# Kernel tuning notes

Hardware: AMD Instinct MI355X
Metric: run time of the kernel (lower is better)

The kernel has to match this reference:

```python
import jax, jax.numpy as jnp
import numpy as np

HEAD_DIM = 256
HIDDEN = 2560
NUM_HEADS = 8
NUM_KV_HEADS = 4
INPUT_DIM = HIDDEN * 2
B, S = 2, 2048


def rotate_half(x):
    x1, x2 = x[..., : x.shape[-1] // 2], x[..., x.shape[-1] // 2 :]
    return jnp.concatenate((-x2, x1), axis=-1)


def setup_inputs() -> dict:
    key = jax.random.key(0)
    ks = jax.random.split(key, 6)
    hidden_states = jax.random.normal(ks[0], (B, S, INPUT_DIM), dtype=jnp.float32)
    # causal additive mask (0 on/below diagonal, large negative above)
    causal = jnp.tril(jnp.ones((S, S), dtype=bool))
    attention_mask = jnp.where(causal, 0.0, -1e9).astype(jnp.float32)
    attention_mask = jnp.broadcast_to(attention_mask[None, None], (B, 1, S, S))
    position_ids = jnp.broadcast_to(jnp.arange(S, dtype=jnp.int32)[None], (B, S))
    sc = 1.0 / np.sqrt(INPUT_DIM)
    Wq = jax.random.normal(ks[1], (NUM_HEADS * HEAD_DIM, INPUT_DIM), dtype=jnp.float32) * sc
    Wk = jax.random.normal(ks[2], (NUM_KV_HEADS * HEAD_DIM, INPUT_DIM), dtype=jnp.float32) * sc
    Wv = jax.random.normal(ks[3], (NUM_KV_HEADS * HEAD_DIM, INPUT_DIM), dtype=jnp.float32) * sc
    Wo = jax.random.normal(ks[4], (HIDDEN, NUM_HEADS * HEAD_DIM), dtype=jnp.float32) * (1.0 / np.sqrt(NUM_HEADS * HEAD_DIM))
    return {"hidden_states": hidden_states, "attention_mask": attention_mask,
            "position_ids": position_ids, "Wq": Wq, "Wk": Wk, "Wv": Wv, "Wo": Wo}


def reference(hidden_states, attention_mask, position_ids, Wq, Wk, Wv, Wo):
    bsz, q_len, _ = hidden_states.shape
    groups = NUM_HEADS // NUM_KV_HEADS
    q = (hidden_states @ Wq.T).reshape(bsz, q_len, NUM_HEADS, HEAD_DIM).transpose(0, 2, 1, 3)
    k = (hidden_states @ Wk.T).reshape(bsz, q_len, NUM_KV_HEADS, HEAD_DIM).transpose(0, 2, 1, 3)
    v = (hidden_states @ Wv.T).reshape(bsz, q_len, NUM_KV_HEADS, HEAD_DIM).transpose(0, 2, 1, 3)
    # RoPE (uses position_ids[0], matching the torch module)
    inv_freq = 1.0 / (10000.0 ** (jnp.arange(0, HEAD_DIM, 2, dtype=jnp.float32) / HEAD_DIM))
    freqs = position_ids[0].astype(jnp.float32)[:, None] * inv_freq[None, :]  # [S, D/2]
    emb = jnp.concatenate((freqs, freqs), axis=-1)  # [S, D]
    cos = jnp.cos(emb)[None, None].astype(q.dtype)
    sin = jnp.sin(emb)[None, None].astype(q.dtype)
    q = q * cos + rotate_half(q) * sin
    k = k * cos + rotate_half(k) * sin
    # GQA: repeat kv heads
    k = jnp.repeat(k, groups, axis=1)  # [B, H, S, D]
    v = jnp.repeat(v, groups, axis=1)
    scores = jnp.einsum("bhqd,bhkd->bhqk", q, k) / np.sqrt(HEAD_DIM)
    scores = scores + attention_mask
    attn = jax.nn.softmax(scores.astype(jnp.float32), axis=-1).astype(q.dtype)
    out = jnp.einsum("bhqk,bhkd->bhqd", attn, v)
    out = out.transpose(0, 2, 1, 3).reshape(bsz, q_len, NUM_HEADS * HEAD_DIM)
    return out @ Wo.T
```

## Files before the change

### kernel.cpp

```cpp
#include <hip/hip_runtime.h>
#include <hip/hip_bf16.h>
#include <cstdint>
#include <cstddef>

typedef __bf16 bf16;
typedef bf16 bf16x4 __attribute__((ext_vector_type(4)));
typedef bf16 bf16x8 __attribute__((ext_vector_type(8)));
typedef float f32x4 __attribute__((ext_vector_type(4)));

#define HEAD_DIM 256
#define NHEADS 8
#define NKV 4
#define BATCH 2
#define SEQ 2048
#define IND 5120
#define HID 2560
#define ROWS (BATCH*SEQ)
#define NQKV 4096
#define CHUNKS_PER_BH 80

__device__ __forceinline__ f32x4 mfma16(bf16x8 a, bf16x8 b, f32x4 c) {
  return __builtin_amdgcn_mfma_f32_16x16x32_bf16(a, b, c, 0, 0, 0);
}

__global__ void cast8(const float* __restrict__ in, bf16* __restrict__ out, int n) {
  int i = (blockIdx.x * 256 + threadIdx.x) * 8;
  if (i >= n) return;
  float4 a = *(const float4*)(in + i);
  float4 b = *(const float4*)(in + i + 4);
  bf16x8 o;
  o[0] = (bf16)a.x; o[1] = (bf16)a.y; o[2] = (bf16)a.z; o[3] = (bf16)a.w;
  o[4] = (bf16)b.x; o[5] = (bf16)b.y; o[6] = (bf16)b.z; o[7] = (bf16)b.w;
  *(bf16x8*)(out + i) = o;
}

template<typename OutT>
__global__ __launch_bounds__(512, 2) void gemm_pipe(const bf16* __restrict__ A,
                                                    const bf16* __restrict__ B,
                                                    OutT* __restrict__ C,
                                                    int M, int N, int K) {
  extern __shared__ bf16 smem[];
  const int tid = threadIdx.x;
  const int lane = tid & 63, w = tid >> 6;
  const int wm = w >> 2, wn = w & 3;
  const int l15 = lane & 15, lg = lane >> 4;
  const int gx = gridDim.x;
  const int nwg = gx * gridDim.y;
  const int id = blockIdx.y * gx + blockIdx.x;
  const int nid = (id & 7) * (nwg >> 3) + (id >> 3);
  const int m0 = (nid / gx) * 256, n0 = (nid % gx) * 256;
  const int NT = K >> 5;

  auto stage = [&](int slot, int kt) {
    bf16* sl = smem + slot * 16384;
    #pragma unroll
    for (int i = 0; i < 2; ++i) {
      int cid = i * 512 + tid;
      int row = cid >> 2;
      int sch = (cid & 3) ^ (row & 3);
      __builtin_amdgcn_global_load_lds(
        (const __attribute__((address_space(1))) void*)(A + (size_t)(m0 + row) * K + kt * 32 + sch * 8),
        (__attribute__((address_space(3))) void*)(sl + cid * 8), 16, 0, 0);
    }
    #pragma unroll
    for (int i = 0; i < 2; ++i) {
      int cid = i * 512 + tid;
      int row = cid >> 2;
      int sch = (cid & 3) ^ (row & 3);
      __builtin_amdgcn_global_load_lds(
        (const __attribute__((address_space(1))) void*)(B + (size_t)(n0 + row) * K + kt * 32 + sch * 8),
        (__attribute__((address_space(3))) void*)(sl + 8192 + cid * 8), 16, 0, 0);
    }
  };

  stage(0, 0); stage(1, 1); stage(2, 2);

  f32x4 acc[8][4] = {};
  for (int t = 0; t < NT; ++t) {
    asm volatile("s_waitcnt vmcnt(8)" ::: "memory");
    __builtin_amdgcn_s_barrier();
    const bf16* sl = smem + (t & 3) * 16384;
    bf16x8 a[8], b[4];
    #pragma unroll
    for (int mi = 0; mi < 8; ++mi) {
      int row = wm * 128 + mi * 16 + l15;
      a[mi] = *(const bf16x8*)&sl[(row * 4 + (lg ^ (row & 3))) * 8];
    }
    #pragma unroll
    for (int ni = 0; ni < 4; ++ni) {
      int row = wn * 64 + ni * 16 + l15;
      b[ni] = *(const bf16x8*)&sl[8192 + (row * 4 + (lg ^ (row & 3))) * 8];
    }
    __builtin_amdgcn_s_setprio(1);
    #pragma unroll
    for (int ni = 0; ni < 2; ++ni)
      #pragma unroll
      for (int mi = 0; mi < 8; ++mi)
        acc[mi][ni] = mfma16(a[mi], b[ni], acc[mi][ni]);
    __builtin_amdgcn_s_setprio(0);
    asm volatile("s_waitcnt lgkmcnt(0)" ::: "memory");
    __builtin_amdgcn_s_barrier();
    int kt = t + 3; if (kt > NT - 1) kt = NT - 1;
    stage((t + 3) & 3, kt);
    __builtin_amdgcn_s_setprio(1);
    #pragma unroll
    for (int ni = 2; ni < 4; ++ni)
      #pragma unroll
      for (int mi = 0; mi < 8; ++mi)
        acc[mi][ni] = mfma16(a[mi], b[ni], acc[mi][ni]);
    __builtin_amdgcn_s_setprio(0);
  }

  #pragma unroll
  for (int mi = 0; mi < 8; ++mi)
    #pragma unroll
    for (int ni = 0; ni < 4; ++ni) {
      int row = m0 + wm * 128 + mi * 16 + lg * 4;
      int col = n0 + wn * 64 + ni * 16 + l15;
      #pragma unroll
      for (int r = 0; r < 4; ++r)
        C[(size_t)(row + r) * N + col] = (OutT)acc[mi][ni][r];
    }
}

__global__ void rope_reorder(const bf16* __restrict__ QKV,
                             bf16* __restrict__ Qr, bf16* __restrict__ Kr) {
  const int row = blockIdx.x;
  const int slot = blockIdx.y;
  const int d = threadIdx.x;
  const int b = row >> 11, s = row & 2047;
  const bool isq = slot < 8;
  const int col0 = isq ? slot * HEAD_DIM : 2048 + (slot - 8) * HEAD_DIM;
  float x1 = (float)QKV[(size_t)row * NQKV + col0 + d];
  float x2 = (float)QKV[(size_t)row * NQKV + col0 + d + 128];
  float invf = exp2f((float)d * (-13.287712379549449f / 128.0f));
  float fr = (float)s * invf;
  float sn, cs;
  sincosf(fr, &sn, &cs);
  bf16* dst = isq ? (Qr + ((size_t)(b * NHEADS + slot) * SEQ + s) * HEAD_DIM)
                  : (Kr + ((size_t)(b * NKV + (slot - 8)) * SEQ + s) * HEAD_DIM);
  dst[d]       = (bf16)(x1 * cs - x2 * sn);
  dst[d + 128] = (bf16)(x2 * cs + x1 * sn);
}

__global__ void v_transpose(const bf16* __restrict__ QKV, bf16* __restrict__ VT) {
  __shared__ bf16 tile[64][66];
  const int bkv = blockIdx.y;
  const int b = bkv >> 2, kv = bkv & 3;
  const int st = blockIdx.x & 31, dt = blockIdx.x >> 5;
  const int s0 = st * 64, d0 = dt * 64;
  const int tj = threadIdx.x & 63, ti = threadIdx.x >> 6;
  for (int i = ti; i < 64; i += 4)
    tile[i][tj] = QKV[(size_t)(b * SEQ + s0 + i) * NQKV + 3072 + kv * HEAD_DIM + d0 + tj];
  __syncthreads();
  for (int i = ti; i < 64; i += 4)
    VT[((size_t)bkv * HEAD_DIM + d0 + i) * SEQ + s0 + tj] = tile[tj][i];
}

__global__ __launch_bounds__(256) void flash_attn(const bf16* __restrict__ Q,
                                                  const bf16* __restrict__ Kp,
                                                  const bf16* __restrict__ VT,
                                                  bf16* __restrict__ Opart,
                                                  float* __restrict__ ML) {
  __shared__ bf16 Ks[64 * 256];
  __shared__ bf16 Vs[256 * 64];
  __shared__ bf16 pbuf[4][16][80];

  const int tid = threadIdx.x, lane = tid & 63, w = tid >> 6;
  const int l15 = lane & 15, lg = lane >> 4;

  const int cid = blockIdx.x;
  const int bh = cid / CHUNKS_PER_BH;
  const int c  = cid - bh * CHUNKS_PER_BH;
  int qt, ki;
  if (c < 8)       { qt = c;                 ki = 0; }
  else if (c < 24) { qt = 8  + ((c - 8) >> 1);  ki = (c - 8)  & 1; }
  else if (c < 48) { qt = 16 + (c - 24) / 3;    ki = (c - 24) % 3; }
  else             { qt = 24 + ((c - 48) >> 2); ki = (c - 48) & 3; }
  const int kb0 = ki * 8;
  const int kb1 = min(kb0 + 8, qt + 1);

  const int b = bh >> 3, h = bh & 7, kvh = h >> 1;
  const int bkv = b * NKV + kvh;
  const int q0 = qt * 64 + w * 16;

  const bf16* Qb = Q + ((size_t)bh * SEQ + q0) * HEAD_DIM;
  bf16x8 qf[8];
  #pragma unroll
  for (int dc = 0; dc < 8; ++dc)
    qf[dc] = *(const bf16x8*)&Qb[l15 * HEAD_DIM + dc * 32 + lg * 8];

  f32x4 oacc[16] = {};
  float m = -1e30f, l = 0.f;

  const bf16* Ksrc = Kp + (size_t)bkv * SEQ * HEAD_DIM;
  const bf16* Vsrc = VT + (size_t)bkv * HEAD_DIM * SEQ;

  for (int kb = kb0; kb < kb1; ++kb) {
    const int kbase = kb * 64;
    __syncthreads();
    #pragma unroll
    for (int i = 0; i < 8; ++i) {
      int id = i * 256 + tid;
      int row = id >> 5, ch = id & 31;
      int sc = ch ^ (row & 7);
      __builtin_amdgcn_global_load_lds(
          (const __attribute__((address_space(1))) void*)(Ksrc + (size_t)(kbase + row) * HEAD_DIM + sc * 8),
          (__attribute__((address_space(3))) void*)(Ks + id * 8), 16, 0, 0);
    }
    #pragma unroll
    for (int i = 0; i < 8; ++i) {
      int id = i * 256 + tid;
      int row = id >> 3, ch = id & 7;
      int sc = ch ^ (row & 7);
      __builtin_amdgcn_global_load_lds(
          (const __attribute__((address_space(1))) void*)(Vsrc + (size_t)row * SEQ + kbase + sc * 8),
          (__attribute__((address_space(3))) void*)(Vs + id * 8), 16, 0, 0);
    }
    __syncthreads();

    f32x4 sacc[4] = {};
    #pragma unroll
    for (int j = 0; j < 4; ++j) {
      const bf16* kl = &Ks[(j * 16 + l15) * HEAD_DIM];
      #pragma unroll
      for (int dc = 0; dc < 8; ++dc) {
        int ch = (dc * 4 + lg) ^ (l15 & 7);
        bf16x8 kf = *(const bf16x8*)&kl[ch * 8];
        sacc[j] = mfma16(kf, qf[dc], sacc[j]);
      }
    }

    float px[4][4];
    const bool need_mask = (kbase + 63 > q0);
    #pragma unroll
    for (int j = 0; j < 4; ++j)
      #pragma unroll
      for (int r = 0; r < 4; ++r) {
        float v = sacc[j][r] * 0.0625f;
        if (need_mask) {
          int kcol = kbase + j * 16 + lg * 4 + r;
          v = (kcol <= q0 + l15) ? v : -1e30f;
        }
        px[j][r] = v;
      }

    float mx = px[0][0];
    #pragma unroll
    for (int j = 0; j < 4; ++j)
      #pragma unroll
      for (int r = 0; r < 4; ++r) mx = fmaxf(mx, px[j][r]);
    mx = fmaxf(mx, __shfl_xor(mx, 16));
    mx = fmaxf(mx, __shfl_xor(mx, 32));
    float mnew = fmaxf(m, mx);
    float alpha = __expf(m - mnew);
    m = mnew;
    float s = 0.f;
    #pragma unroll
    for (int j = 0; j < 4; ++j) {
      bf16x4 pk;
      #pragma unroll
      for (int r = 0; r < 4; ++r) {
        float e = __expf(px[j][r] - mnew);
        s += e;
        pk[r] = (bf16)e;
      }
      *(bf16x4*)&pbuf[w][l15][j * 16 + lg * 4] = pk;
    }
    s += __shfl_xor(s, 16);
    s += __shfl_xor(s, 32);
    l = l * alpha + s;

    float ar[4];
    #pragma unroll
    for (int r = 0; r < 4; ++r) ar[r] = __shfl(alpha, lg * 4 + r);
    #pragma unroll
    for (int ni = 0; ni < 16; ++ni)
      #pragma unroll
      for (int r = 0; r < 4; ++r) oacc[ni][r] *= ar[r];

    bf16x8 pa0 = *(const bf16x8*)&pbuf[w][l15][lg * 8];
    bf16x8 pa1 = *(const bf16x8*)&pbuf[w][l15][32 + lg * 8];
    #pragma unroll
    for (int ni = 0; ni < 16; ++ni) {
      const bf16* vb = &Vs[(ni * 16 + l15) * 64];
      int c0 = lg ^ (l15 & 7);
      int c1 = (4 + lg) ^ (l15 & 7);
      bf16x8 v0 = *(const bf16x8*)&vb[c0 * 8];
      bf16x8 v1 = *(const bf16x8*)&vb[c1 * 8];
      oacc[ni] = mfma16(pa0, v0, oacc[ni]);
      oacc[ni] = mfma16(pa1, v1, oacc[ni]);
    }
  }

  bf16* Ob = Opart + ((size_t)cid * 64 + w * 16) * HEAD_DIM;
  #pragma unroll
  for (int ni = 0; ni < 16; ++ni)
    #pragma unroll
    for (int r = 0; r < 4; ++r)
      Ob[(size_t)(lg * 4 + r) * HEAD_DIM + ni * 16 + l15] = (bf16)oacc[ni][r];
  if (lg == 0) {
    ML[((size_t)cid * 64 + w * 16 + l15) * 2]     = m;
    ML[((size_t)cid * 64 + w * 16 + l15) * 2 + 1] = l;
  }
}

__global__ __launch_bounds__(256) void flash_merge(const bf16* __restrict__ Opart,
                                                   const float* __restrict__ ML,
                                                   bf16* __restrict__ AO) {
  const int bh = blockIdx.x, qt = blockIdx.y;
  const int b = bh >> 3, h = bh & 7;
  int cbase, nc;
  if (qt < 8)       { cbase = qt;                nc = 1; }
  else if (qt < 16) { cbase = 8  + 2 * (qt - 8);  nc = 2; }
  else if (qt < 24) { cbase = 24 + 3 * (qt - 16); nc = 3; }
  else              { cbase = 48 + 4 * (qt - 24); nc = 4; }
  const int cid0 = bh * CHUNKS_PER_BH + cbase;

  const int tid = threadIdx.x;
  const int row = tid >> 2, dseg = (tid & 3) * 64;

  float mi[4], li[4];
  float M = -1e30f;
  for (int i = 0; i < nc; ++i) {
    mi[i] = ML[((size_t)(cid0 + i) * 64 + row) * 2];
    li[i] = ML[((size_t)(cid0 + i) * 64 + row) * 2 + 1];
    M = fmaxf(M, mi[i]);
  }
  float wgt[4], L = 0.f;
  for (int i = 0; i < nc; ++i) {
    wgt[i] = __expf(mi[i] - M);
    L += li[i] * wgt[i];
  }
  const float inv = 1.0f / L;

  bf16* dst = AO + ((size_t)(b * SEQ + qt * 64 + row)) * 2048 + h * HEAD_DIM + dseg;
  for (int dv = 0; dv < 8; ++dv) {
    float acc[8] = {};
    for (int i = 0; i < nc; ++i) {
      bf16x8 o = *(const bf16x8*)&Opart[((size_t)(cid0 + i) * 64 + row) * HEAD_DIM + dseg + dv * 8];
      #pragma unroll
      for (int e = 0; e < 8; ++e) acc[e] += wgt[i] * (float)o[e];
    }
    bf16x8 ov;
    #pragma unroll
    for (int e = 0; e < 8; ++e) ov[e] = (bf16)(acc[e] * inv);
    *(bf16x8*)&dst[dv * 8] = ov;
  }
}

extern "C" void kernel_launch(void* const* d_in, const int* in_sizes, int n_in,
                              void* d_out, int out_size, void* d_ws, size_t ws_size,
                              hipStream_t stream) {
  const float* hs = (const float*)d_in[0];
  const float* Wq = (const float*)d_in[3];
  const float* Wk = (const float*)d_in[4];
  const float* Wv = (const float*)d_in[5];
  const float* Wo = (const float*)d_in[6];
  float* out = (float*)d_out;

  char* ws = (char*)d_ws;
  bf16* hsb  = (bf16*)(ws);
  bf16* wqkv = (bf16*)(ws + 41943040);
  bf16* qkv  = (bf16*)(ws + 83886080);
  bf16* qr   = (bf16*)(ws + 117440512);
  bf16* kr   = (bf16*)(ws + 134217728);
  bf16* vt   = (bf16*)(ws + 142606336);
  bf16* ao   = (bf16*)(ws + 150994944);
  bf16* wob  = (bf16*)(ws + 167772160);
  bf16*  opart = (bf16*)(ws);
  float* ml    = (float*)(ws + 41943040);

  hipFuncSetAttribute((const void*)&gemm_pipe<bf16>,  hipFuncAttributeMaxDynamicSharedMemorySize, 131072);
  hipFuncSetAttribute((const void*)&gemm_pipe<float>, hipFuncAttributeMaxDynamicSharedMemorySize, 131072);

  cast8<<<ROWS * IND / 2048, 256, 0, stream>>>(hs, hsb, ROWS * IND);
  cast8<<<2048 * IND / 2048, 256, 0, stream>>>(Wq, wqkv, 2048 * IND);
  cast8<<<1024 * IND / 2048, 256, 0, stream>>>(Wk, wqkv + 2048 * IND, 1024 * IND);
  cast8<<<1024 * IND / 2048, 256, 0, stream>>>(Wv, wqkv + 3072 * IND, 1024 * IND);
  cast8<<<HID * 2048 / 2048, 256, 0, stream>>>(Wo, wob, HID * 2048);

  gemm_pipe<bf16><<<dim3(NQKV / 256, ROWS / 256), 512, 131072, stream>>>(hsb, wqkv, qkv, ROWS, NQKV, IND);

  rope_reorder<<<dim3(ROWS, 12), 128, 0, stream>>>(qkv, qr, kr);
  v_transpose<<<dim3(128, BATCH * NKV), 256, 0, stream>>>(qkv, vt);

  flash_attn<<<dim3(16 * CHUNKS_PER_BH), 256, 0, stream>>>(qr, kr, vt, opart, ml);
  flash_merge<<<dim3(16, 32), 256, 0, stream>>>(opart, ml, ao);

  gemm_pipe<float><<<dim3(HID / 256, ROWS / 256), 512, 131072, stream>>>(ao, wob, out, ROWS, HID, 2048);
}
```

Measured before the change: 443.9 us.

## Double-buffer LDS fragment reads in GEMM and fuse cast kernels into one launch

The GEMM main loop is restructured so each iteration reads the next K-slice's fragments from shared memory into a second register set while MFMAs run on the current set. A single barrier per K step replaces the previous two, with a sched_barrier fence and a relaxed vmcnt wait. Separately, the five fp32-to-bf16 cast launches are merged into one kernel that dispatches on the flat index. This removes launch overhead and LDS-read latency stalls, at the cost of more VGPRs for the extra fragment set, which may hurt occupancy under launch_bounds(512,2).

```diff
diff --git a/kernel.cpp b/kernel.cpp
--- a/kernel.cpp
+++ b/kernel.cpp
@@ -23,15 +23,23 @@
   return __builtin_amdgcn_mfma_f32_16x16x32_bf16(a, b, c, 0, 0, 0);
 }
 
-__global__ void cast8(const float* __restrict__ in, bf16* __restrict__ out, int n) {
-  int i = (blockIdx.x * 256 + threadIdx.x) * 8;
-  if (i >= n) return;
-  float4 a = *(const float4*)(in + i);
-  float4 b = *(const float4*)(in + i + 4);
+__global__ void cast_all(const float* __restrict__ hs, const float* __restrict__ wq,
+                         const float* __restrict__ wk, const float* __restrict__ wv,
+                         const float* __restrict__ wo,
+                         bf16* __restrict__ dst01, bf16* __restrict__ dwo) {
+  long i = ((long)blockIdx.x * 256 + threadIdx.x) * 8;
+  const float* src; bf16* dst;
+  if (i < 20971520L)      { src = hs + i;              dst = dst01 + i; }
+  else if (i < 31457280L) { src = wq + (i - 20971520); dst = dst01 + i; }
+  else if (i < 36700160L) { src = wk + (i - 31457280); dst = dst01 + i; }
+  else if (i < 41943040L) { src = wv + (i - 36700160); dst = dst01 + i; }
+  else                    { src = wo + (i - 41943040); dst = dwo + (i - 41943040); }
+  float4 a = *(const float4*)(src);
+  float4 b = *(const float4*)(src + 4);
   bf16x8 o;
   o[0] = (bf16)a.x; o[1] = (bf16)a.y; o[2] = (bf16)a.z; o[3] = (bf16)a.w;
   o[4] = (bf16)b.x; o[5] = (bf16)b.y; o[6] = (bf16)b.z; o[7] = (bf16)b.w;
-  *(bf16x8*)(out + i) = o;
+  *(bf16x8*)dst = o;
 }
 
 template<typename OutT>
@@ -73,43 +81,56 @@
     }
   };
 
-  stage(0, 0); stage(1, 1); stage(2, 2);
+  const int ach = lg ^ (l15 & 3);
+  const int aoff = ((wm * 128 + l15) * 4 + ach) * 8;
+  const int boff = 8192 + ((wn * 64 + l15) * 4 + ach) * 8;
+
+  auto read_slot = [&](const bf16* sl, bf16x8 (&a)[8], bf16x8 (&b)[4]) {
+    #pragma unroll
+    for (int mi = 0; mi < 8; ++mi) a[mi] = *(const bf16x8*)&sl[aoff + mi * 512];
+    #pragma unroll
+    for (int ni = 0; ni < 4; ++ni) b[ni] = *(const bf16x8*)&sl[boff + ni * 512];
+  };
 
   f32x4 acc[8][4] = {};
-  for (int t = 0; t < NT; ++t) {
-    asm volatile("s_waitcnt vmcnt(8)" ::: "memory");
-    __builtin_amdgcn_s_barrier();
-    const bf16* sl = smem + (t & 3) * 16384;
-    bf16x8 a[8], b[4];
-    #pragma unroll
-    for (int mi = 0; mi < 8; ++mi) {
-      int row = wm * 128 + mi * 16 + l15;
-      a[mi] = *(const bf16x8*)&sl[(row * 4 + (lg ^ (row & 3))) * 8];
-    }
-    #pragma unroll
-    for (int ni = 0; ni < 4; ++ni) {
-      int row = wn * 64 + ni * 16 + l15;
-      b[ni] = *(const bf16x8*)&sl[8192 + (row * 4 + (lg ^ (row & 3))) * 8];
-    }
+  auto domfma = [&](bf16x8 (&a)[8], bf16x8 (&b)[4]) {
     __builtin_amdgcn_s_setprio(1);
     #pragma unroll
-    for (int ni = 0; ni < 2; ++ni)
+    for (int ni = 0; ni < 4; ++ni)
       #pragma unroll
       for (int mi = 0; mi < 8; ++mi)
         acc[mi][ni] = mfma16(a[mi], b[ni], acc[mi][ni]);
     __builtin_amdgcn_s_setprio(0);
-    asm volatile("s_waitcnt lgkmcnt(0)" ::: "memory");
+  };
+
+  bf16x8 aE[8], bE[4], aO[8], bO[4];
+  stage(0, 0); stage(1, 1); stage(2, 2);
+  asm volatile("s_waitcnt vmcnt(8)" ::: "memory");
+  __builtin_amdgcn_s_barrier();
+  __builtin_amdgcn_sched_barrier(0);
+  read_slot(smem, aE, bE);
+
+  int t = 0;
+  for (; t < NT - 2; t += 2) {
+    asm volatile("s_waitcnt vmcnt(4)" ::: "memory");
     __builtin_amdgcn_s_barrier();
-    int kt = t + 3; if (kt > NT - 1) kt = NT - 1;
-    stage((t + 3) & 3, kt);
-    __builtin_amdgcn_s_setprio(1);
-    #pragma unroll
-    for (int ni = 2; ni < 4; ++ni)
-      #pragma unroll
-      for (int mi = 0; mi < 8; ++mi)
-        acc[mi][ni] = mfma16(a[mi], b[ni], acc[mi][ni]);
-    __builtin_amdgcn_s_setprio(0);
-  }
+    __builtin_amdgcn_sched_barrier(0);
+    read_slot(smem + ((t + 1) & 3) * 16384, aO, bO);
+    { int kt = t + 3; if (kt > NT - 1) kt = NT - 1; stage((t + 3) & 3, kt); }
+    domfma(aE, bE);
+    asm volatile("s_waitcnt vmcnt(4)" ::: "memory");
+    __builtin_amdgcn_s_barrier();
+    __builtin_amdgcn_sched_barrier(0);
+    read_slot(smem + ((t + 2) & 3) * 16384, aE, bE);
+    { int kt = t + 4; if (kt > NT - 1) kt = NT - 1; stage((t + 4) & 3, kt); }
+    domfma(aO, bO);
+  }
+  asm volatile("s_waitcnt vmcnt(4)" ::: "memory");
+  __builtin_amdgcn_s_barrier();
+  __builtin_amdgcn_sched_barrier(0);
+  read_slot(smem + ((NT - 1) & 3) * 16384, aO, bO);
+  domfma(aE, bE);
+  domfma(aO, bO);
 
   #pragma unroll
   for (int mi = 0; mi < 8; ++mi)
@@ -374,11 +395,7 @@
   hipFuncSetAttribute((const void*)&gemm_pipe<bf16>,  hipFuncAttributeMaxDynamicSharedMemorySize, 131072);
   hipFuncSetAttribute((const void*)&gemm_pipe<float>, hipFuncAttributeMaxDynamicSharedMemorySize, 131072);
 
-  cast8<<<ROWS * IND / 2048, 256, 0, stream>>>(hs, hsb, ROWS * IND);
-  cast8<<<2048 * IND / 2048, 256, 0, stream>>>(Wq, wqkv, 2048 * IND);
-  cast8<<<1024 * IND / 2048, 256, 0, stream>>>(Wk, wqkv + 2048 * IND, 1024 * IND);
-  cast8<<<1024 * IND / 2048, 256, 0, stream>>>(Wv, wqkv + 3072 * IND, 1024 * IND);
-  cast8<<<HID * 2048 / 2048, 256, 0, stream>>>(Wo, wob, HID * 2048);
+  cast_all<<<23040, 256, 0, stream>>>(hs, Wq, Wk, Wv, Wo, (bf16*)ws, wob);
 
   gemm_pipe<bf16><<<dim3(NQKV / 256, ROWS / 256), 512, 131072, stream>>>(hsb, wqkv, qkv, ROWS, NQKV, IND);
 
```

Measured after the change: 415.7 us. -6.4%, faster.
